# Performance work log

Measured on AMD Instinct MI355X. Metric: run time of the kernel, lower is better.

Reference implementation:

```python
import jax, jax.numpy as jnp
import numpy as np

GROUP_SIZE = 64

def _dequant_w4(qweight, wscales):
    """Unpack int4 weights and apply per-(group, out-channel) scales.
    qweight: [N, K//2] uint8-valued ints, low nibble = even k, high nibble = odd k.
    wscales: [K//GROUP_SIZE, N] float. Returns [N, K] float weight.
    """
    q = qweight.astype(jnp.int32)
    low = (q & 15) - 8          # [N, K//2], signed int4
    high = ((q >> 4) & 15) - 8  # [N, K//2]
    N = q.shape[0]
    K = q.shape[1] * 2
    w_int = jnp.stack([low, high], axis=-1).reshape(N, K)  # interleaved low/high
    # scale[n, k] = wscales[k // GROUP_SIZE, n]
    scale = jnp.repeat(wscales, GROUP_SIZE, axis=0).T  # [N, K]
    return w_int.astype(wscales.dtype) * scale

def setup_inputs() -> dict:
    key = jax.random.key(0)
    ks = jax.random.split(key, 7)
    M, K, N, R = 8192, 4096, 4096, 32
    x = jax.random.normal(ks[0], (M, K), dtype=jnp.float32)
    qweight = jax.random.randint(ks[1], (N, K // 2), 0, 256, dtype=jnp.int32)
    wscales = jax.random.uniform(ks[2], (K // GROUP_SIZE, N), dtype=jnp.float32) * 0.01 + 0.001
    proj_down = jax.random.normal(ks[3], (R, K), dtype=jnp.float32) * 0.02
    proj_up = jax.random.normal(ks[4], (N, R), dtype=jnp.float32) * 0.02
    wtscale = jnp.ones((1,), dtype=jnp.float32)
    bias = jax.random.normal(ks[5], (N,), dtype=jnp.float32) * 0.01
    return {"x": x, "qweight": qweight, "wscales": wscales,
            "proj_down": proj_down, "proj_up": proj_up,
            "wtscale": wtscale, "bias": bias}

def reference(x, qweight, wscales, proj_down, proj_up, wtscale, bias):
    # Dequant int4 weight, GEMM, low-rank LoRA correction scaled by wtscale, bias.
    w = _dequant_w4(qweight, wscales)              # [N, K]
    out = x @ w.T                                  # [M, N]
    lora = (x @ proj_down.T) @ proj_up.T           # [M, R] @ [R, N] -> [M, N]
    out = out + lora * wtscale
    out = out + bias
    return out
```

## Files before the change

kernel.cpp:

```cpp
#include <hip/hip_runtime.h>
#include <hip/hip_bf16.h>
#include <stdint.h>

#define MD 8192
#define ND 4096
#define KD 4096
#define RD 32

typedef __bf16 bf16x8 __attribute__((ext_vector_type(8)));
typedef float f32x4 __attribute__((ext_vector_type(4)));

__device__ __forceinline__ void cp16(const void* g, void* l) {
    __builtin_amdgcn_global_load_lds(
        (const __attribute__((address_space(1))) void*)g,
        (__attribute__((address_space(3))) void*)l, 16, 0, 0);
}

__global__ __launch_bounds__(256) void cvt_x(const float* __restrict__ x,
                                             __hip_bfloat16* __restrict__ y) {
    size_t i = ((size_t)blockIdx.x * 256 + threadIdx.x) * 8;
    float4 a = *(const float4*)(x + i);
    float4 b = *(const float4*)(x + i + 4);
    union { __hip_bfloat16 h[8]; uint4 u; } o;
    o.h[0] = __float2bfloat16(a.x); o.h[1] = __float2bfloat16(a.y);
    o.h[2] = __float2bfloat16(a.z); o.h[3] = __float2bfloat16(a.w);
    o.h[4] = __float2bfloat16(b.x); o.h[5] = __float2bfloat16(b.y);
    o.h[6] = __float2bfloat16(b.z); o.h[7] = __float2bfloat16(b.w);
    *(uint4*)(y + i) = o.u;
}

__global__ __launch_bounds__(256) void build_weff(
    const int* __restrict__ qw,
    const float* __restrict__ wsc,
    const float* __restrict__ pd,
    const float* __restrict__ pu,
    const float* __restrict__ wts_p,
    __hip_bfloat16* __restrict__ weff)
{
    __shared__ float pd_s[RD][128];
    __shared__ float pu_t[RD][64];
    const int t = threadIdx.x;
    const int kb = blockIdx.x * 128;
    const int nb = blockIdx.y * 64;

    for (int f = t; f < (RD * 128) / 4; f += 256) {
        int r = f >> 5;
        int c = (f & 31) << 2;
        *(float4*)&pd_s[r][c] = *(const float4*)(pd + (size_t)r * KD + kb + c);
    }
    for (int f = t; f < (64 * RD) / 4; f += 256) {
        int nl = f >> 3;
        int r4 = (f & 7) << 2;
        float4 v = *(const float4*)(pu + (size_t)(nb + nl) * RD + r4);
        pu_t[r4 + 0][nl] = v.x; pu_t[r4 + 1][nl] = v.y;
        pu_t[r4 + 2][nl] = v.z; pu_t[r4 + 3][nl] = v.w;
    }
    __syncthreads();

    const float wts = wts_p[0];
    const int kc = (t & 31) << 2;
    const int ng = (t >> 5) << 3;

    float acc[8][4];
#pragma unroll
    for (int i = 0; i < 8; ++i)
#pragma unroll
        for (int j = 0; j < 4; ++j) acc[i][j] = 0.f;

    for (int r = 0; r < RD; ++r) {
        float4 pdv = *(const float4*)&pd_s[r][kc];
        float4 pua = *(const float4*)&pu_t[r][ng];
        float4 pub = *(const float4*)&pu_t[r][ng + 4];
        float pus[8] = {pua.x, pua.y, pua.z, pua.w, pub.x, pub.y, pub.z, pub.w};
#pragma unroll
        for (int i = 0; i < 8; ++i) {
            acc[i][0] += pus[i] * pdv.x;
            acc[i][1] += pus[i] * pdv.y;
            acc[i][2] += pus[i] * pdv.z;
            acc[i][3] += pus[i] * pdv.w;
        }
    }

    const int kg = kb + kc;
    const int g = kg >> 6;
#pragma unroll
    for (int i = 0; i < 8; ++i) {
        const int n = nb + ng + i;
        const float sc = wsc[(size_t)g * ND + n];
        int2 q = *(const int2*)(qw + (size_t)n * (KD / 2) + (kg >> 1));
        const int w0 = (q.x & 15) - 8;
        const int w1 = ((q.x >> 4) & 15) - 8;
        const int w2 = (q.y & 15) - 8;
        const int w3 = ((q.y >> 4) & 15) - 8;
        union { __hip_bfloat16 h[4]; uint2 u; } o;
        o.h[0] = __float2bfloat16((float)w0 * sc + wts * acc[i][0]);
        o.h[1] = __float2bfloat16((float)w1 * sc + wts * acc[i][1]);
        o.h[2] = __float2bfloat16((float)w2 * sc + wts * acc[i][2]);
        o.h[3] = __float2bfloat16((float)w3 * sc + wts * acc[i][3]);
        *(uint2*)(weff + (size_t)n * KD + kg) = o.u;
    }
}

__global__ __launch_bounds__(256) void gemm_bt_bias(
    const __hip_bfloat16* __restrict__ A,
    const __hip_bfloat16* __restrict__ B,
    const float* __restrict__ bias,
    float* __restrict__ C)
{
    __shared__ alignas(16) __hip_bfloat16 As[128 * 32];
    __shared__ alignas(16) __hip_bfloat16 Bs[128 * 32];

    const int t = threadIdx.x;
    const int lane = t & 63;
    const int wave = t >> 6;
    const int wr = wave >> 1;
    const int wc = wave & 1;
    const int m0 = blockIdx.y * 128;
    const int n0 = blockIdx.x * 128;

    const int srow = t >> 2;
    const int scol = (t & 3) * 8;
    const __hip_bfloat16* Ag = A + (size_t)(m0 + srow) * KD + scol;
    const __hip_bfloat16* Bg = B + (size_t)(n0 + srow) * KD + scol;
    char* AsB = (char*)As + wave * 1024;
    char* BsB = (char*)Bs + wave * 1024;

    const int qm = lane & 15;
    const int ko = (lane >> 4) * 8;

    f32x4 acc[4][4];
#pragma unroll
    for (int i = 0; i < 4; ++i)
#pragma unroll
        for (int j = 0; j < 4; ++j) acc[i][j] = (f32x4){0.f, 0.f, 0.f, 0.f};

    for (int kt = 0; kt < KD; kt += 32) {
        cp16(Ag + kt, AsB);
        cp16(Ag + kt + 64 * KD, AsB + 4096);
        cp16(Bg + kt, BsB);
        cp16(Bg + kt + 64 * KD, BsB + 4096);
        __syncthreads();

        bf16x8 af[4], bfr[4];
#pragma unroll
        for (int i = 0; i < 4; ++i)
            af[i] = *(const bf16x8*)(As + (wr * 64 + i * 16 + qm) * 32 + ko);
#pragma unroll
        for (int j = 0; j < 4; ++j)
            bfr[j] = *(const bf16x8*)(Bs + (wc * 64 + j * 16 + qm) * 32 + ko);

#pragma unroll
        for (int i = 0; i < 4; ++i)
#pragma unroll
            for (int j = 0; j < 4; ++j)
                acc[i][j] = __builtin_amdgcn_mfma_f32_16x16x32_bf16(
                    af[i], bfr[j], acc[i][j], 0, 0, 0);
        __syncthreads();
    }

    const int cm0 = (lane >> 4) * 4;
    const int cn = lane & 15;
#pragma unroll
    for (int j = 0; j < 4; ++j) {
        const int n = n0 + wc * 64 + j * 16 + cn;
        const float bv = bias[n];
#pragma unroll
        for (int i = 0; i < 4; ++i) {
            const int mr = m0 + wr * 64 + i * 16 + cm0;
            float* dst = C + (size_t)mr * ND + n;
#pragma unroll
            for (int r = 0; r < 4; ++r)
                dst[(size_t)r * ND] = acc[i][j][r] + bv;
        }
    }
}

extern "C" void kernel_launch(void* const* d_in, const int* in_sizes, int n_in,
                              void* d_out, int out_size, void* d_ws, size_t ws_size,
                              hipStream_t stream) {
    const float* x    = (const float*)d_in[0];
    const int* qw     = (const int*)d_in[1];
    const float* wsc  = (const float*)d_in[2];
    const float* pd   = (const float*)d_in[3];
    const float* pu   = (const float*)d_in[4];
    const float* wts  = (const float*)d_in[5];
    const float* bias = (const float*)d_in[6];
    float* out = (float*)d_out;

    __hip_bfloat16* weff = (__hip_bfloat16*)d_ws;
    __hip_bfloat16* xbf  = (__hip_bfloat16*)((char*)d_ws + (size_t)ND * KD * sizeof(__hip_bfloat16));

    cvt_x<<<(MD * (size_t)KD) / (256 * 8), 256, 0, stream>>>(x, xbf);
    build_weff<<<dim3(KD / 128, ND / 64), 256, 0, stream>>>(qw, wsc, pd, pu, wts, weff);
    gemm_bt_bias<<<dim3(ND / 128, MD / 128), 256, 0, stream>>>(xbf, weff, bias, out);
}
```

Before: 560.4 us.

## Swizzle GEMM LDS layout, remap block order for XCDs, widen weff stores

The GEMM now XOR-swizzles the 16-byte column chunks of each LDS row, both when staging global loads and when reading MFMA fragments, to reduce LDS bank conflicts. It also uses a 1D grid with a remapped block-to-tile order so that consecutive blocks spread across N tiles, aiming for better L2 reuse across XCDs. build_weff gives each thread 8 contiguous k values with 128-bit loads and stores, and pads its shared arrays. The swizzle has to match exactly on the store and load sides, and the tile remap changes the cache access pattern.

```diff
diff --git a/kernel.cpp b/kernel.cpp
--- a/kernel.cpp
+++ b/kernel.cpp
@@ -37,8 +37,8 @@
     const float* __restrict__ wts_p,
     __hip_bfloat16* __restrict__ weff)
 {
-    __shared__ float pd_s[RD][128];
-    __shared__ float pu_t[RD][64];
+    __shared__ float pd_s[RD][132];
+    __shared__ float pu_t[RD][68];
     const int t = threadIdx.x;
     const int kb = blockIdx.x * 128;
     const int nb = blockIdx.y * 64;
@@ -58,46 +58,45 @@
     __syncthreads();
 
     const float wts = wts_p[0];
-    const int kc = (t & 31) << 2;
-    const int ng = (t >> 5) << 3;
+    const int kc = (t & 15) << 3;
+    const int ng = (t >> 4) << 2;
 
-    float acc[8][4];
+    float acc[4][8];
 #pragma unroll
-    for (int i = 0; i < 8; ++i)
+    for (int i = 0; i < 4; ++i)
 #pragma unroll
-        for (int j = 0; j < 4; ++j) acc[i][j] = 0.f;
+        for (int j = 0; j < 8; ++j) acc[i][j] = 0.f;
 
     for (int r = 0; r < RD; ++r) {
-        float4 pdv = *(const float4*)&pd_s[r][kc];
-        float4 pua = *(const float4*)&pu_t[r][ng];
-        float4 pub = *(const float4*)&pu_t[r][ng + 4];
-        float pus[8] = {pua.x, pua.y, pua.z, pua.w, pub.x, pub.y, pub.z, pub.w};
+        float4 pda = *(const float4*)&pd_s[r][kc];
+        float4 pdb = *(const float4*)&pd_s[r][kc + 4];
+        float4 puv = *(const float4*)&pu_t[r][ng];
+        float pus[4] = {puv.x, puv.y, puv.z, puv.w};
+        float pdv[8] = {pda.x, pda.y, pda.z, pda.w, pdb.x, pdb.y, pdb.z, pdb.w};
 #pragma unroll
-        for (int i = 0; i < 8; ++i) {
-            acc[i][0] += pus[i] * pdv.x;
-            acc[i][1] += pus[i] * pdv.y;
-            acc[i][2] += pus[i] * pdv.z;
-            acc[i][3] += pus[i] * pdv.w;
-        }
+        for (int i = 0; i < 4; ++i)
+#pragma unroll
+            for (int j = 0; j < 8; ++j)
+                acc[i][j] += pus[i] * pdv[j];
     }
 
     const int kg = kb + kc;
     const int g = kg >> 6;
 #pragma unroll
-    for (int i = 0; i < 8; ++i) {
+    for (int i = 0; i < 4; ++i) {
         const int n = nb + ng + i;
         const float sc = wsc[(size_t)g * ND + n];
-        int2 q = *(const int2*)(qw + (size_t)n * (KD / 2) + (kg >> 1));
-        const int w0 = (q.x & 15) - 8;
-        const int w1 = ((q.x >> 4) & 15) - 8;
-        const int w2 = (q.y & 15) - 8;
-        const int w3 = ((q.y >> 4) & 15) - 8;
-        union { __hip_bfloat16 h[4]; uint2 u; } o;
-        o.h[0] = __float2bfloat16((float)w0 * sc + wts * acc[i][0]);
-        o.h[1] = __float2bfloat16((float)w1 * sc + wts * acc[i][1]);
-        o.h[2] = __float2bfloat16((float)w2 * sc + wts * acc[i][2]);
-        o.h[3] = __float2bfloat16((float)w3 * sc + wts * acc[i][3]);
-        *(uint2*)(weff + (size_t)n * KD + kg) = o.u;
+        int4 q = *(const int4*)(qw + (size_t)n * (KD / 2) + (kg >> 1));
+        const int qi[4] = {q.x, q.y, q.z, q.w};
+        union { __hip_bfloat16 h[8]; uint4 u; } o;
+#pragma unroll
+        for (int j = 0; j < 4; ++j) {
+            const int lo = (qi[j] & 15) - 8;
+            const int hi = ((qi[j] >> 4) & 15) - 8;
+            o.h[2 * j]     = __float2bfloat16((float)lo * sc + wts * acc[i][2 * j]);
+            o.h[2 * j + 1] = __float2bfloat16((float)hi * sc + wts * acc[i][2 * j + 1]);
+        }
+        *(uint4*)(weff + (size_t)n * KD + kg) = o.u;
     }
 }
 
@@ -115,18 +114,22 @@
     const int wave = t >> 6;
     const int wr = wave >> 1;
     const int wc = wave & 1;
-    const int m0 = blockIdx.y * 128;
-    const int n0 = blockIdx.x * 128;
+
+    const int bid = blockIdx.x;
+    const int nb = (bid & 7) * 4 + ((bid >> 3) & 3);
+    const int mb = bid >> 5;
+    const int m0 = mb * 128;
+    const int n0 = nb * 128;
 
     const int srow = t >> 2;
-    const int scol = (t & 3) * 8;
+    const int scol = ((t & 3) ^ ((t >> 3) & 3)) * 8;
     const __hip_bfloat16* Ag = A + (size_t)(m0 + srow) * KD + scol;
     const __hip_bfloat16* Bg = B + (size_t)(n0 + srow) * KD + scol;
     char* AsB = (char*)As + wave * 1024;
     char* BsB = (char*)Bs + wave * 1024;
 
     const int qm = lane & 15;
-    const int ko = (lane >> 4) * 8;
+    const int ko_sw = (((lane >> 4) ^ ((qm >> 1) & 3))) * 8;
 
     f32x4 acc[4][4];
 #pragma unroll
@@ -144,10 +147,10 @@
         bf16x8 af[4], bfr[4];
 #pragma unroll
         for (int i = 0; i < 4; ++i)
-            af[i] = *(const bf16x8*)(As + (wr * 64 + i * 16 + qm) * 32 + ko);
+            af[i] = *(const bf16x8*)(As + (wr * 64 + i * 16 + qm) * 32 + ko_sw);
 #pragma unroll
         for (int j = 0; j < 4; ++j)
-            bfr[j] = *(const bf16x8*)(Bs + (wc * 64 + j * 16 + qm) * 32 + ko);
+            bfr[j] = *(const bf16x8*)(Bs + (wc * 64 + j * 16 + qm) * 32 + ko_sw);
 
 #pragma unroll
         for (int i = 0; i < 4; ++i)
@@ -192,5 +195,5 @@
 
     cvt_x<<<(MD * (size_t)KD) / (256 * 8), 256, 0, stream>>>(x, xbf);
     build_weff<<<dim3(KD / 128, ND / 64), 256, 0, stream>>>(qw, wsc, pd, pu, wts, weff);
-    gemm_bt_bias<<<dim3(ND / 128, MD / 128), 256, 0, stream>>>(xbf, weff, bias, out);
+    gemm_bt_bias<<<2048, 256, 0, stream>>>(xbf, weff, bias, out);
 }
```

Result: no change. 565.0 us (+0.8%).
